# Performance work log

Measured on AMD Instinct MI355X. Metric: run time of the kernel, lower is better.

## Reference

```python
import jax, jax.numpy as jnp
import numpy as np

B, S, D, H = 2, 2048, 2048, 16
DH = D // H  # 128
ROPE_BASE = 10000.0


def setup_inputs() -> dict:
    key = jax.random.key(0)
    ks = jax.random.split(key, 5)
    scale = 0.02
    return {
        "x": jax.random.normal(ks[0], (B, S, D), dtype=jnp.float32),
        "wq": jax.random.normal(ks[1], (D, D), dtype=jnp.float32) * scale,
        "wk": jax.random.normal(ks[2], (D, D), dtype=jnp.float32) * scale,
        "wv": jax.random.normal(ks[3], (D, D), dtype=jnp.float32) * scale,
        "wo": jax.random.normal(ks[4], (D, D), dtype=jnp.float32) * scale,
    }


def _rope_cache(seq_len, dhead):
    # flash-attn RotaryEmbedding: inv_freq over even dims, full rotary_dim = dhead
    inv_freq = 1.0 / (ROPE_BASE ** (jnp.arange(0, dhead, 2, dtype=jnp.float32) / dhead))
    t = jnp.arange(seq_len, dtype=jnp.float32)
    freqs = jnp.einsum("s,d->sd", t, inv_freq)  # [S, DH/2]
    return jnp.cos(freqs), jnp.sin(freqs)


def _apply_rope_interleaved(t, cos, sin):
    # t: [B, S, H, DH]; interleaved pairs (t[...,0::2], t[...,1::2])
    te, to = t[..., 0::2], t[..., 1::2]
    c = cos[None, :, None, :]
    s = sin[None, :, None, :]
    re = te * c - to * s
    ro = te * s + to * c
    return jnp.stack([re, ro], axis=-1).reshape(t.shape)


def reference(x, wq, wk, wv, wo):
    b, s, d = x.shape
    q = (x @ wq).reshape(b, s, H, DH)
    k = (x @ wk).reshape(b, s, H, DH)
    v = (x @ wv).reshape(b, s, H, DH)

    cos, sin = _rope_cache(s, DH)
    q = _apply_rope_interleaved(q.astype(jnp.float32), cos, sin)
    k = _apply_rope_interleaved(k.astype(jnp.float32), cos, sin)

    # flash_attn_func(causal=True) semantics: bf16 inputs, fp32 softmax, scale 1/sqrt(dhead)
    qb = q.astype(jnp.bfloat16)
    kb = k.astype(jnp.bfloat16)
    vb = v.astype(jnp.bfloat16)
    scale = 1.0 / np.sqrt(DH)
    scores = jnp.einsum("bqhd,bkhd->bhqk", qb, kb,
                        preferred_element_type=jnp.float32) * scale
    causal = jnp.tril(jnp.ones((s, s), dtype=bool))
    scores = jnp.where(causal[None, None], scores, -jnp.inf)
    p = jax.nn.softmax(scores, axis=-1)  # fp32
    attn = jnp.einsum("bhqk,bkhd->bqhd", p.astype(jnp.bfloat16), vb,
                      preferred_element_type=jnp.float32)
    attn = attn.astype(jnp.bfloat16).astype(x.dtype)  # flash returns bf16, then .to(x)
    out = attn.reshape(b, s, d) @ wo
    return out
```

## Files before the change

### kernel.cpp

```cpp
#include <hip/hip_runtime.h>
#include <hip/hip_bf16.h>
#include <stdint.h>

#define B_SZ   2
#define S_LEN  2048
#define DMODEL 2048
#define NH     16
#define DHD    128

typedef __attribute__((ext_vector_type(8))) __bf16 bf16x8;
typedef __attribute__((ext_vector_type(4))) float  f32x4;
typedef __attribute__((ext_vector_type(4))) float  float4v;
typedef __attribute__((ext_vector_type(8))) unsigned short ushort8;
typedef __attribute__((ext_vector_type(4))) unsigned short ushort4v;

__device__ __forceinline__ unsigned short f2bf(float f) {
  unsigned int u = __float_as_uint(f);
  unsigned int r = (u + 0x7fffu + ((u >> 16) & 1u)) >> 16;
  return (unsigned short)r;
}

__device__ __forceinline__ unsigned int cvt_pk_bf16(float lo, float hi) {
  unsigned int r;
  asm("v_cvt_pk_bf16_f32 %0, %1, %2" : "=v"(r) : "v"(lo), "v"(hi));
  return r;
}

__device__ __forceinline__ void async_cp16(void* lds, const void* g) {
  __builtin_amdgcn_global_load_lds(
      (const __attribute__((address_space(1))) void*)g,
      (__attribute__((address_space(3))) void*)lds, 16, 0, 0);
}

__global__ __launch_bounds__(256) void k_prep(const float* __restrict__ in,
                                              unsigned short* __restrict__ out,
                                              float* __restrict__ cosT,
                                              float* __restrict__ sinT) {
  const int bx = blockIdx.x;
  const int t = threadIdx.x;
  if (bx < 8192) {
    int i = bx * 256 + t;
    float4v v = ((const float4v*)in)[i];
    ushort4v o;
    o[0] = f2bf(v[0]); o[1] = f2bf(v[1]); o[2] = f2bf(v[2]); o[3] = f2bf(v[3]);
    ((ushort4v*)out)[i] = o;
  } else {
    int i = (bx - 8192) * 256 + t;
    int s = i >> 6, dj = i & 63;
    float e = __expf(-9.210340371976184f * (float)dj * (1.0f / 64.0f));
    float f = (float)s * e;
    cosT[i] = cosf(f);
    sinT[i] = sinf(f);
  }
}

__global__ __launch_bounds__(256) void k_transpose_all(const float* __restrict__ w0,
                                                       const float* __restrict__ w1,
                                                       const float* __restrict__ w2,
                                                       const float* __restrict__ w3,
                                                       unsigned short* __restrict__ WTbase) {
  __shared__ unsigned short tile[64 * 72];
  const int z = blockIdx.z;
  const float* W = (z == 0) ? w0 : (z == 1) ? w1 : (z == 2) ? w2 : w3;
  unsigned short* WT = WTbase + (size_t)z * 4194304;
  const int n0 = blockIdx.x * 64;
  const int k0 = blockIdx.y * 64;
  const int t = threadIdx.x;
#pragma unroll
  for (int i = 0; i < 4; ++i) {
    int c = t + 256 * i;
    int r = c >> 4, c4 = c & 15;
    float4v v = *(const float4v*)(W + (size_t)(k0 + r) * DMODEL + n0 + c4 * 4);
    ushort4v o;
    o[0] = f2bf(v[0]); o[1] = f2bf(v[1]); o[2] = f2bf(v[2]); o[3] = f2bf(v[3]);
    *(ushort4v*)(&tile[r * 72 + c4 * 4]) = o;
  }
  __syncthreads();
#pragma unroll
  for (int i = 0; i < 2; ++i) {
    int c = t + 256 * i;
    int n = c >> 3, k8 = c & 7;
    ushort8 o;
#pragma unroll
    for (int j = 0; j < 8; ++j) o[j] = tile[(k8 * 8 + j) * 72 + n];
    *(ushort8*)(WT + (size_t)(n0 + n) * DMODEL + k0 + k8 * 8) = o;
  }
}

template <int EPI>
__global__ __launch_bounds__(512, 2) void k_gemm128(
    const unsigned short* __restrict__ A,
    const unsigned short* __restrict__ BT,
    float* __restrict__ C0,
    unsigned short* __restrict__ Cq,
    unsigned short* __restrict__ Ck,
    unsigned short* __restrict__ Cv,
    const float* __restrict__ cosT,
    const float* __restrict__ sinT,
    int chn) {
  __shared__ char smem[98304];
  const int tid = threadIdx.x;

  const int xcd = blockIdx.x & 7;
  const int idx = blockIdx.x >> 3;
  const int bm = (xcd >> 2) * 16 + (idx & 15);
  const int bn = (xcd & 3) * chn + (idx >> 4);

  const int gs = (tid & 7) ^ ((tid >> 3) & 7);
  const unsigned short* Abase = A + (size_t)(bm * 128 + (tid >> 3)) * 2048 + gs * 8;
  const unsigned short* Bbase = BT + (size_t)(bn * 256 + (tid >> 3)) * 2048 + gs * 8;
  const int dstA = tid * 16;
  const int dstB = 16384 + tid * 16;

  const int lane = tid & 63, wid = tid >> 6;
  const int wr = wid >> 2, wcn = wid & 3;
  const int lr = lane & 15, hi = lane >> 4;
  int aoff[4][2], boff[4][2];
#pragma unroll
  for (int m = 0; m < 4; ++m) {
    int row = wr * 64 + m * 16 + lr;
#pragma unroll
    for (int k = 0; k < 2; ++k)
      aoff[m][k] = row * 128 + ((((k * 4 + hi)) ^ (row & 7)) << 4);
  }
#pragma unroll
  for (int n = 0; n < 4; ++n) {
    int row = wcn * 64 + n * 16 + lr;
#pragma unroll
    for (int k = 0; k < 2; ++k)
      boff[n][k] = 16384 + row * 128 + ((((k * 4 + hi)) ^ (row & 7)) << 4);
  }

  f32x4 acc[4][4];
#pragma unroll
  for (int m = 0; m < 4; ++m)
#pragma unroll
    for (int n = 0; n < 4; ++n) {
      f32x4 z = {0.f, 0.f, 0.f, 0.f};
      acc[m][n] = z;
    }

#define STG_A(c, t_) do {                                                   \
    const unsigned short* _s = Abase + (t_) * 64;                           \
    async_cp16(smem + (c) * 49152 + dstA, _s);                              \
    async_cp16(smem + (c) * 49152 + dstA + 8192, _s + 64 * 2048);           \
  } while (0)
#define STG_B(c, t_) do {                                                   \
    const unsigned short* _s = Bbase + (t_) * 64;                           \
    async_cp16(smem + (c) * 49152 + dstB, _s);                              \
    async_cp16(smem + (c) * 49152 + dstB + 8192, _s + 64 * 2048);           \
    async_cp16(smem + (c) * 49152 + dstB + 16384, _s + 128 * 2048);         \
    async_cp16(smem + (c) * 49152 + dstB + 24576, _s + 192 * 2048);         \
  } while (0)

  auto tile = [&](int T, int CC, bool DO_A, bool DO_B, int VM) __attribute__((always_inline)) {
    const char* Sb = smem + CC * 49152;
    bf16x8 a0[4], b0[4], a1[4], b1[4];
#pragma unroll
    for (int m = 0; m < 4; ++m) a0[m] = *(const bf16x8*)(Sb + aoff[m][0]);
#pragma unroll
    for (int n = 0; n < 4; ++n) b0[n] = *(const bf16x8*)(Sb + boff[n][0]);
    if (DO_A) STG_A(CC ^ 1, T + 1);
    asm volatile("s_waitcnt lgkmcnt(0)" ::: "memory");
    __builtin_amdgcn_sched_barrier(0);
    __builtin_amdgcn_s_setprio(1);
#pragma unroll
    for (int m = 0; m < 4; ++m) {
      acc[m][0] = __builtin_amdgcn_mfma_f32_16x16x32_bf16(a0[m], b0[0], acc[m][0], 0, 0, 0);
      acc[m][1] = __builtin_amdgcn_mfma_f32_16x16x32_bf16(a0[m], b0[1], acc[m][1], 0, 0, 0);
    }
    __builtin_amdgcn_s_setprio(0);
    __builtin_amdgcn_sched_barrier(0);
#pragma unroll
    for (int m = 0; m < 4; ++m) a1[m] = *(const bf16x8*)(Sb + aoff[m][1]);
#pragma unroll
    for (int n = 0; n < 4; ++n) b1[n] = *(const bf16x8*)(Sb + boff[n][1]);
    __builtin_amdgcn_sched_barrier(0);
    __builtin_amdgcn_s_setprio(1);
#pragma unroll
    for (int m = 0; m < 4; ++m) {
      acc[m][2] = __builtin_amdgcn_mfma_f32_16x16x32_bf16(a0[m], b0[2], acc[m][2], 0, 0, 0);
      acc[m][3] = __builtin_amdgcn_mfma_f32_16x16x32_bf16(a0[m], b0[3], acc[m][3], 0, 0, 0);
    }
    __builtin_amdgcn_s_setprio(0);
    __builtin_amdgcn_s_barrier();
    __builtin_amdgcn_sched_barrier(0);
    asm volatile("s_waitcnt lgkmcnt(0)" ::: "memory");
    __builtin_amdgcn_sched_barrier(0);
    if (DO_B) STG_B(CC, T + 2);
    __builtin_amdgcn_s_setprio(1);
#pragma unroll
    for (int m = 0; m < 4; ++m)
#pragma unroll
      for (int n = 0; n < 4; ++n)
        acc[m][n] = __builtin_amdgcn_mfma_f32_16x16x32_bf16(a1[m], b1[n], acc[m][n], 0, 0, 0);
    __builtin_amdgcn_s_setprio(0);
    if (VM == 0) asm volatile("s_waitcnt vmcnt(4)" ::: "memory");
    else if (VM == 1) asm volatile("s_waitcnt vmcnt(0)" ::: "memory");
    if (VM != 2) {
      __builtin_amdgcn_s_barrier();
      __builtin_amdgcn_sched_barrier(0);
    }
  };

  STG_B(0, 0);
  STG_A(0, 0);
  STG_B(1, 1);
  asm volatile("s_waitcnt vmcnt(4)" ::: "memory");
  __builtin_amdgcn_s_barrier();
  __builtin_amdgcn_sched_barrier(0);

  for (int it = 0; it < 15; ++it) {
    tile(2 * it, 0, true, true, 0);
    tile(2 * it + 1, 1, true, true, 0);
  }
  tile(30, 0, true, false, 1);
  tile(31, 1, false, false, 2);

  const int row_b = bm * 128 + wr * 64 + hi * 4;
  const int col_b = bn * 256 + wcn * 64 + lr;
  if (EPI == 0) {
#pragma unroll
    for (int m = 0; m < 4; ++m)
#pragma unroll
      for (int n = 0; n < 4; ++n) {
        int col = col_b + n * 16;
#pragma unroll
        for (int j = 0; j < 4; ++j) {
          int row = row_b + m * 16 + j;
          C0[(size_t)row * 2048 + col] = acc[m][n][j];
        }
      }
  } else {
    const int sel = bn >> 3;
#pragma unroll
    for (int m = 0; m < 4; ++m) {
#pragma unroll
      for (int n = 0; n < 4; ++n) {
        int col = col_b + n * 16;
        int hh = (col >> 7) & 15, d = col & 127;
        if (sel == 2) {
#pragma unroll
          for (int j = 0; j < 4; ++j) {
            int row = row_b + m * 16 + j;
            int b = row >> 11, s = row & 2047;
            Cv[((size_t)(b * NH + hh) * S_LEN + s) * DHD + d] = f2bf(acc[m][n][j]);
          }
        } else {
          unsigned short* dst = sel ? Ck : Cq;
          int dj = d >> 1;
          float sgn = (d & 1) ? 1.f : -1.f;
#pragma unroll
          for (int j = 0; j < 4; ++j) {
            int row = row_b + m * 16 + j;
            int b = row >> 11, s = row & 2047;
            float v = acc[m][n][j];
            float pp = __shfl_xor(v, 1);
            float cc = cosT[(s << 6) + dj];
            float sn = sinT[(s << 6) + dj];
            dst[((size_t)(b * NH + hh) * S_LEN + s) * DHD + d] = f2bf(v * cc + sgn * pp * sn);
          }
        }
      }
    }
  }
#undef STG_A
#undef STG_B
}

__global__ __launch_bounds__(256) void k_flash_attn(const unsigned short* __restrict__ Qg,
                                                    const unsigned short* __restrict__ Kg,
                                                    const unsigned short* __restrict__ Vg,
                                                    unsigned short* __restrict__ Og) {
  __shared__ unsigned short K_lds[2][64 * 128];
  __shared__ unsigned short VT_lds[2][128 * 64];

  const int lid = blockIdx.x;
  const int pq = (lid >> 3) & 15;
  const int hb = ((lid >> 7) << 3) | (lid & 7);
  const int h = hb & 15, b = hb >> 4;

  const int t = threadIdx.x;
  const int lane = t & 63, wave = t >> 6;
  const int hi = lane >> 4, lr = lane & 15;

  const size_t head = (size_t)(b * NH + h) * (size_t)(S_LEN * DHD);
  const unsigned short* Q = Qg + head;
  const unsigned short* Kp = Kg + head;
  const unsigned short* Vp = Vg + head;

  const int kr0 = t >> 4;
  const int kgc = (t & 15) ^ (kr0 & 7);
  const unsigned short* Kbase = Kp + (size_t)kr0 * DHD + kgc * 8;
  const int kdst = t * 16;

  const int vdc = t & 15, vsp0 = t >> 4;
  const unsigned short* Vbase = Vp + (size_t)(2 * vsp0) * DHD + vdc * 8;
  const int bo0 = 16 * ((vsp0 >> 1) & 3) + 8 * ((vsp0 >> 3) & 1) + 4 * (vsp0 & 1);

  const float sc = 0.08838834764831845f;

  for (int pass = 0; pass < 2; ++pass) {
    const int qt = (pass == 0) ? pq : (31 - pq);
    const int nt = qt + 1;
    const int qbase = qt * 64 + wave * 16;
    const int qrow = qbase + lr;

    bf16x8 qf[4];
    {
      const unsigned short* qr_ = Q + (size_t)(qbase + lr) * DHD;
#pragma unroll
      for (int kc = 0; kc < 4; ++kc) qf[kc] = *(const bf16x8*)(qr_ + kc * 32 + hi * 8);
    }

    f32x4 of[8];
#pragma unroll
    for (int i = 0; i < 8; ++i) {
      f32x4 z = {0.f, 0.f, 0.f, 0.f};
      of[i] = z;
    }
    float mS = -INFINITY;
    float lsum = 0.f;

    {
#pragma unroll
      for (int i = 0; i < 4; ++i)
        async_cp16((char*)K_lds[0] + kdst + i * 4096, Kbase + (size_t)(16 * i) * DHD);
      ushort8 va0 = *(const ushort8*)(Vbase);
      ushort8 vb0 = *(const ushort8*)(Vbase + DHD);
      ushort8 va1 = *(const ushort8*)(Vbase + (size_t)32 * DHD);
      ushort8 vb1 = *(const ushort8*)(Vbase + (size_t)33 * DHD);
#pragma unroll
      for (int j = 0; j < 8; ++j) {
        int row = vdc * 8 + j;
        int swz = ((j ^ vdc) & 7) << 4;
        *(unsigned int*)((char*)VT_lds[0] + row * 128 + (bo0 ^ swz)) =
            (unsigned int)va0[j] | ((unsigned int)vb0[j] << 16);
        *(unsigned int*)((char*)VT_lds[0] + row * 128 + ((bo0 | 64) ^ swz)) =
            (unsigned int)va1[j] | ((unsigned int)vb1[j] << 16);
      }
    }
    __syncthreads();

    for (int tt = 0; tt < nt; ++tt) {
      const int cur = tt & 1;
      const int kv0 = tt * 64;
      const bool more = (tt + 1 < nt);
      const bool diag = (tt == qt);

      ushort8 va0, vb0, va1, vb1;
      if (more) {
        const unsigned short* ks = Kbase + (size_t)(kv0 + 64) * DHD;
#pragma unroll
        for (int i = 0; i < 4; ++i)
          async_cp16((char*)K_lds[cur ^ 1] + kdst + i * 4096, ks + (size_t)(16 * i) * DHD);
        const unsigned short* vs = Vbase + (size_t)(kv0 + 64) * DHD;
        va0 = *(const ushort8*)(vs);
        vb0 = *(const ushort8*)(vs + DHD);
        va1 = *(const ushort8*)(vs + (size_t)32 * DHD);
        vb1 = *(const ushort8*)(vs + (size_t)33 * DHD);
      }

      const char* Kb = (const char*)K_lds[cur];
      f32x4 sf[4];
#pragma unroll
      for (int n = 0; n < 4; ++n) {
        f32x4 z = {0.f, 0.f, 0.f, 0.f};
        sf[n] = z;
      }
      __builtin_amdgcn_s_setprio(1);
#pragma unroll
      for (int n = 0; n < 4; ++n) {
        const int kr = n * 16 + lr;
        const int kswz = (kr & 7) << 4;
#pragma unroll
        for (int kc = 0; kc < 4; ++kc) {
          bf16x8 kf = *(const bf16x8*)(Kb + kr * 256 + ((kc * 64 + hi * 16) ^ kswz));
          sf[n] = __builtin_amdgcn_mfma_f32_16x16x32_bf16(kf, qf[kc], sf[n], 0, 0, 0);
        }
      }
      __builtin_amdgcn_s_setprio(0);

      float p[4][4];
      float mx = -INFINITY;
      if (diag) {
#pragma unroll
        for (int n = 0; n < 4; ++n)
#pragma unroll
          for (int j = 0; j < 4; ++j) {
            int kvcol = kv0 + n * 16 + hi * 4 + j;
            float v = (kvcol > qrow) ? -INFINITY : sf[n][j];
            p[n][j] = v;
            mx = fmaxf(mx, v);
          }
      } else {
#pragma unroll
        for (int n = 0; n < 4; ++n)
#pragma unroll
          for (int j = 0; j < 4; ++j) {
            float v = sf[n][j];
            p[n][j] = v;
            mx = fmaxf(mx, v);
          }
      }
      mx = fmaxf(mx, __shfl_xor(mx, 16));
      mx = fmaxf(mx, __shfl_xor(mx, 32));
      float mn = fmaxf(mS, mx);
      float corr = __expf((mS - mn) * sc);
      mS = mn;
      float mns = mn * sc;
      float rs = 0.f;
#pragma unroll
      for (int n = 0; n < 4; ++n)
#pragma unroll
        for (int j = 0; j < 4; ++j) {
          float e = __expf(__builtin_fmaf(p[n][j], sc, -mns));
          p[n][j] = e;
          rs += e;
        }
      rs += __shfl_xor(rs, 16);
      rs += __shfl_xor(rs, 32);
      lsum = lsum * corr + rs;

      unsigned int pk[4][2];
#pragma unroll
      for (int n = 0; n < 4; ++n) {
        pk[n][0] = cvt_pk_bf16(p[n][0], p[n][1]);
        pk[n][1] = cvt_pk_bf16(p[n][2], p[n][3]);
      }

      float corrb[4];
#pragma unroll
      for (int j = 0; j < 4; ++j) corrb[j] = __shfl(corr, hi * 4 + j);
#pragma unroll
      for (int nd = 0; nd < 8; ++nd)
#pragma unroll
        for (int j = 0; j < 4; ++j) of[nd][j] *= corrb[j];

      const char* Vb = (const char*)VT_lds[cur];
      __builtin_amdgcn_s_setprio(1);
#pragma unroll
      for (int kc = 0; kc < 2; ++kc) {
        union { unsigned int u[4]; bf16x8 v; } pa;
        pa.u[0] = pk[2 * kc][0];
        pa.u[1] = pk[2 * kc][1];
        pa.u[2] = pk[2 * kc + 1][0];
        pa.u[3] = pk[2 * kc + 1][1];
#pragma unroll
        for (int nd = 0; nd < 8; ++nd) {
          const int vr = nd * 16 + lr;
          const int vswz = ((vr & 7) ^ ((vr >> 3) & 7)) << 4;
          bf16x8 vf = *(const bf16x8*)(Vb + vr * 128 + ((kc * 64 + hi * 16) ^ vswz));
          of[nd] = __builtin_amdgcn_mfma_f32_16x16x32_bf16(pa.v, vf, of[nd], 0, 0, 0);
        }
      }
      __builtin_amdgcn_s_setprio(0);

      if (more) {
        char* Vw = (char*)VT_lds[cur ^ 1];
#pragma unroll
        for (int j = 0; j < 8; ++j) {
          int row = vdc * 8 + j;
          int swz = ((j ^ vdc) & 7) << 4;
          *(unsigned int*)(Vw + row * 128 + (bo0 ^ swz)) =
              (unsigned int)va0[j] | ((unsigned int)vb0[j] << 16);
          *(unsigned int*)(Vw + row * 128 + ((bo0 | 64) ^ swz)) =
              (unsigned int)va1[j] | ((unsigned int)vb1[j] << 16);
        }
      }
      __syncthreads();
    }

    float inv[4];
#pragma unroll
    for (int j = 0; j < 4; ++j) {
      float ls = __shfl(lsum, hi * 4 + j);
      inv[j] = 1.0f / ls;
    }
#pragma unroll
    for (int nd = 0; nd < 8; ++nd)
#pragma unroll
      for (int j = 0; j < 4; ++j) {
        int qr = qbase + hi * 4 + j;
        Og[((size_t)(b * S_LEN + qr) * NH + h) * DHD + nd * 16 + lr] = f2bf(of[nd][j] * inv[j]);
      }
  }
}

extern "C" void kernel_launch(void* const* d_in, const int* in_sizes, int n_in,
                              void* d_out, int out_size, void* d_ws, size_t ws_size,
                              hipStream_t stream) {
  const float* x  = (const float*)d_in[0];
  const float* wq = (const float*)d_in[1];
  const float* wk = (const float*)d_in[2];
  const float* wv = (const float*)d_in[3];
  const float* wo = (const float*)d_in[4];
  float* out = (float*)d_out;

  char* ws = (char*)d_ws;
  unsigned short* xb    = (unsigned short*)(ws);
  unsigned short* wqT   = (unsigned short*)(ws + 16777216);
  unsigned short* woT   = (unsigned short*)(ws + 41943040);
  unsigned short* qb    = (unsigned short*)(ws + 50331648);
  unsigned short* kb    = (unsigned short*)(ws + 67108864);
  unsigned short* vb    = (unsigned short*)(ws + 83886080);
  float*          cosT  = (float*)(ws + 100663296);
  float*          sinT  = (float*)(ws + 101187584);
  unsigned short* attnb = xb;

  k_prep<<<8704, 256, 0, stream>>>(x, xb, cosT, sinT);
  dim3 tg(32, 32, 4);
  k_transpose_all<<<tg, 256, 0, stream>>>(wq, wk, wv, wo, wqT);

  k_gemm128<1><<<768, 512, 0, stream>>>(xb, wqT, nullptr, qb, kb, vb, cosT, sinT, 6);

  k_flash_attn<<<512, 256, 0, stream>>>(qb, kb, vb, attnb);

  k_gemm128<0><<<256, 512, 0, stream>>>(attnb, woT, out, nullptr, nullptr, nullptr,
                                        nullptr, nullptr, 2);
}
```

Measured before the change: 229.1 us.

## Use 256x384 tiles for QKV GEMM and merge prep with weight transpose

New measurement: 238.4 us. +4.0%, slower.

```diff
diff --git a/kernel.cpp b/kernel.cpp
--- a/kernel.cpp
+++ b/kernel.cpp
@@ -32,20 +32,52 @@
       (__attribute__((address_space(3))) void*)lds, 16, 0, 0);
 }
 
-__global__ __launch_bounds__(256) void k_prep(const float* __restrict__ in,
-                                              unsigned short* __restrict__ out,
-                                              float* __restrict__ cosT,
-                                              float* __restrict__ sinT) {
+__global__ __launch_bounds__(256) void k_prep_all(const float* __restrict__ x,
+                                                  const float* __restrict__ w0,
+                                                  const float* __restrict__ w1,
+                                                  const float* __restrict__ w2,
+                                                  const float* __restrict__ w3,
+                                                  unsigned short* __restrict__ xb,
+                                                  unsigned short* __restrict__ WTbase,
+                                                  float* __restrict__ cosT,
+                                                  float* __restrict__ sinT) {
+  __shared__ unsigned short tile[64 * 72];
   const int bx = blockIdx.x;
   const int t = threadIdx.x;
-  if (bx < 8192) {
-    int i = bx * 256 + t;
-    float4v v = ((const float4v*)in)[i];
+  if (bx < 4096) {
+    const int z = bx >> 10;
+    const int wi = bx & 1023;
+    const float* W = (z == 0) ? w0 : (z == 1) ? w1 : (z == 2) ? w2 : w3;
+    unsigned short* WT = WTbase + (size_t)z * 4194304;
+    const int n0 = (wi & 31) * 64;
+    const int k0 = (wi >> 5) * 64;
+#pragma unroll
+    for (int i = 0; i < 4; ++i) {
+      int c = t + 256 * i;
+      int r = c >> 4, c4 = c & 15;
+      float4v v = *(const float4v*)(W + (size_t)(k0 + r) * DMODEL + n0 + c4 * 4);
+      ushort4v o;
+      o[0] = f2bf(v[0]); o[1] = f2bf(v[1]); o[2] = f2bf(v[2]); o[3] = f2bf(v[3]);
+      *(ushort4v*)(&tile[r * 72 + c4 * 4]) = o;
+    }
+    __syncthreads();
+#pragma unroll
+    for (int i = 0; i < 2; ++i) {
+      int c = t + 256 * i;
+      int n = c >> 3, k8 = c & 7;
+      ushort8 o;
+#pragma unroll
+      for (int j = 0; j < 8; ++j) o[j] = tile[(k8 * 8 + j) * 72 + n];
+      *(ushort8*)(WT + (size_t)(n0 + n) * DMODEL + k0 + k8 * 8) = o;
+    }
+  } else if (bx < 12288) {
+    int i = (bx - 4096) * 256 + t;
+    float4v v = ((const float4v*)x)[i];
     ushort4v o;
     o[0] = f2bf(v[0]); o[1] = f2bf(v[1]); o[2] = f2bf(v[2]); o[3] = f2bf(v[3]);
-    ((ushort4v*)out)[i] = o;
+    ((ushort4v*)xb)[i] = o;
   } else {
-    int i = (bx - 8192) * 256 + t;
+    int i = (bx - 12288) * 256 + t;
     int s = i >> 6, dj = i & 63;
     float e = __expf(-9.210340371976184f * (float)dj * (1.0f / 64.0f));
     float f = (float)s * e;
@@ -54,49 +86,150 @@
   }
 }
 
-__global__ __launch_bounds__(256) void k_transpose_all(const float* __restrict__ w0,
-                                                       const float* __restrict__ w1,
-                                                       const float* __restrict__ w2,
-                                                       const float* __restrict__ w3,
-                                                       unsigned short* __restrict__ WTbase) {
-  __shared__ unsigned short tile[64 * 72];
-  const int z = blockIdx.z;
-  const float* W = (z == 0) ? w0 : (z == 1) ? w1 : (z == 2) ? w2 : w3;
-  unsigned short* WT = WTbase + (size_t)z * 4194304;
-  const int n0 = blockIdx.x * 64;
-  const int k0 = blockIdx.y * 64;
-  const int t = threadIdx.x;
-#pragma unroll
-  for (int i = 0; i < 4; ++i) {
-    int c = t + 256 * i;
-    int r = c >> 4, c4 = c & 15;
-    float4v v = *(const float4v*)(W + (size_t)(k0 + r) * DMODEL + n0 + c4 * 4);
-    ushort4v o;
-    o[0] = f2bf(v[0]); o[1] = f2bf(v[1]); o[2] = f2bf(v[2]); o[3] = f2bf(v[3]);
-    *(ushort4v*)(&tile[r * 72 + c4 * 4]) = o;
-  }
-  __syncthreads();
-#pragma unroll
-  for (int i = 0; i < 2; ++i) {
-    int c = t + 256 * i;
-    int n = c >> 3, k8 = c & 7;
-    ushort8 o;
-#pragma unroll
-    for (int j = 0; j < 8; ++j) o[j] = tile[(k8 * 8 + j) * 72 + n];
-    *(ushort8*)(WT + (size_t)(n0 + n) * DMODEL + k0 + k8 * 8) = o;
-  }
-}
-
-template <int EPI>
-__global__ __launch_bounds__(512, 2) void k_gemm128(
+__global__ __launch_bounds__(512, 1) void k_gemm_qkv(
     const unsigned short* __restrict__ A,
     const unsigned short* __restrict__ BT,
-    float* __restrict__ C0,
     unsigned short* __restrict__ Cq,
     unsigned short* __restrict__ Ck,
     unsigned short* __restrict__ Cv,
     const float* __restrict__ cosT,
-    const float* __restrict__ sinT,
+    const float* __restrict__ sinT) {
+  __shared__ char smem[122880];
+  const int tid = threadIdx.x;
+
+  const int xcd = blockIdx.x & 7;
+  const int idx = blockIdx.x >> 3;
+  const int bm = (xcd >> 1) * 4 + (idx & 3);
+  const int bn = (xcd & 1) * 8 + (idx >> 2);
+
+  const int r0 = tid >> 2;
+  const int gs = (tid & 3) ^ (r0 & 3);
+  const unsigned short* Abase = A + (size_t)(bm * 256 + r0) * 2048 + gs * 8;
+  const unsigned short* Bbase = BT + (size_t)(bn * 384 + r0) * 2048 + gs * 8;
+  const int dstA = tid * 16;
+  const int dstB = 16384 + tid * 16;
+
+  const int lane = tid & 63, wid = tid >> 6;
+  const int wr = wid >> 2, wcn = wid & 3;
+  const int lr = lane & 15, hi = lane >> 4;
+  const int swz = (hi ^ (lr & 3)) << 4;
+  const int aB = (wr * 128 + lr) * 64 + swz;
+  const int bB = 16384 + (wcn * 96 + lr) * 64 + swz;
+
+  f32x4 acc[8][6];
+#pragma unroll
+  for (int m = 0; m < 8; ++m)
+#pragma unroll
+    for (int n = 0; n < 6; ++n) {
+      f32x4 z = {0.f, 0.f, 0.f, 0.f};
+      acc[m][n] = z;
+    }
+
+#define STG(c, t_) do {                                                     \
+    const unsigned short* _a = Abase + (t_) * 32;                           \
+    async_cp16(smem + (c) * 40960 + dstA, _a);                              \
+    async_cp16(smem + (c) * 40960 + dstA + 8192, _a + (size_t)128 * 2048);  \
+    const unsigned short* _b = Bbase + (t_) * 32;                           \
+    async_cp16(smem + (c) * 40960 + dstB, _b);                              \
+    async_cp16(smem + (c) * 40960 + dstB + 8192, _b + (size_t)128 * 2048);  \
+    async_cp16(smem + (c) * 40960 + dstB + 16384, _b + (size_t)256 * 2048); \
+  } while (0)
+
+  auto tile = [&](int T, int CC) __attribute__((always_inline)) {
+    const char* Sb = smem + CC * 40960;
+    if (T + 2 < 64) {
+      const int nc = (CC + 2 >= 3) ? (CC - 1) : (CC + 2);
+      STG(nc, T + 2);
+    }
+    bf16x8 b0[6], a0[4];
+#pragma unroll
+    for (int n = 0; n < 6; ++n) b0[n] = *(const bf16x8*)(Sb + bB + n * 1024);
+#pragma unroll
+    for (int m = 0; m < 4; ++m) a0[m] = *(const bf16x8*)(Sb + aB + m * 1024);
+    asm volatile("s_waitcnt lgkmcnt(0)" ::: "memory");
+    __builtin_amdgcn_sched_barrier(0);
+    __builtin_amdgcn_s_setprio(1);
+#pragma unroll
+    for (int m = 0; m < 4; ++m)
+#pragma unroll
+      for (int n = 0; n < 6; ++n)
+        acc[m][n] = __builtin_amdgcn_mfma_f32_16x16x32_bf16(a0[m], b0[n], acc[m][n], 0, 0, 0);
+    __builtin_amdgcn_s_setprio(0);
+    __builtin_amdgcn_sched_barrier(0);
+    bf16x8 a1[4];
+#pragma unroll
+    for (int m = 0; m < 4; ++m) a1[m] = *(const bf16x8*)(Sb + aB + (m + 4) * 1024);
+    asm volatile("s_waitcnt lgkmcnt(0)" ::: "memory");
+    __builtin_amdgcn_sched_barrier(0);
+    __builtin_amdgcn_s_setprio(1);
+#pragma unroll
+    for (int m = 0; m < 4; ++m)
+#pragma unroll
+      for (int n = 0; n < 6; ++n)
+        acc[m + 4][n] = __builtin_amdgcn_mfma_f32_16x16x32_bf16(a1[m], b0[n], acc[m + 4][n], 0, 0, 0);
+    __builtin_amdgcn_s_setprio(0);
+    if (T < 62) asm volatile("s_waitcnt vmcnt(5)" ::: "memory");
+    else if (T == 62) asm volatile("s_waitcnt vmcnt(0)" ::: "memory");
+    if (T < 63) {
+      __builtin_amdgcn_s_barrier();
+      __builtin_amdgcn_sched_barrier(0);
+    }
+  };
+
+  STG(0, 0);
+  STG(1, 1);
+  asm volatile("s_waitcnt vmcnt(5)" ::: "memory");
+  __builtin_amdgcn_s_barrier();
+  __builtin_amdgcn_sched_barrier(0);
+
+  for (int it = 0; it < 21; ++it) {
+    tile(3 * it, 0);
+    tile(3 * it + 1, 1);
+    tile(3 * it + 2, 2);
+  }
+  tile(63, 0);
+
+  const int row_b = bm * 256 + wr * 128 + hi * 4;
+  const int col_b = bn * 384 + wcn * 96 + lr;
+#pragma unroll
+  for (int n = 0; n < 6; ++n) {
+    const int col = col_b + n * 16;
+    const int sel = col >> 11;
+    const int hh = (col >> 7) & 15, d = col & 127;
+    if (sel == 2) {
+#pragma unroll
+      for (int m = 0; m < 8; ++m)
+#pragma unroll
+        for (int j = 0; j < 4; ++j) {
+          int row = row_b + m * 16 + j;
+          int b = row >> 11, s = row & 2047;
+          Cv[((size_t)(b * NH + hh) * S_LEN + s) * DHD + d] = f2bf(acc[m][n][j]);
+        }
+    } else {
+      unsigned short* dst = sel ? Ck : Cq;
+      const int dj = d >> 1;
+      const float sgn = (d & 1) ? 1.f : -1.f;
+#pragma unroll
+      for (int m = 0; m < 8; ++m)
+#pragma unroll
+        for (int j = 0; j < 4; ++j) {
+          int row = row_b + m * 16 + j;
+          int b = row >> 11, s = row & 2047;
+          float v = acc[m][n][j];
+          float pp = __shfl_xor(v, 1);
+          float cc = cosT[(s << 6) + dj];
+          float sn = sinT[(s << 6) + dj];
+          dst[((size_t)(b * NH + hh) * S_LEN + s) * DHD + d] = f2bf(v * cc + sgn * pp * sn);
+        }
+    }
+  }
+#undef STG
+}
+
+__global__ __launch_bounds__(512, 2) void k_gemm_wo(
+    const unsigned short* __restrict__ A,
+    const unsigned short* __restrict__ BT,
+    float* __restrict__ C0,
     int chn) {
   __shared__ char smem[98304];
   const int tid = threadIdx.x;
@@ -219,51 +352,17 @@
 
   const int row_b = bm * 128 + wr * 64 + hi * 4;
   const int col_b = bn * 256 + wcn * 64 + lr;
-  if (EPI == 0) {
-#pragma unroll
-    for (int m = 0; m < 4; ++m)
-#pragma unroll
-      for (int n = 0; n < 4; ++n) {
-        int col = col_b + n * 16;
-#pragma unroll
-        for (int j = 0; j < 4; ++j) {
-          int row = row_b + m * 16 + j;
-          C0[(size_t)row * 2048 + col] = acc[m][n][j];
-        }
-      }
-  } else {
-    const int sel = bn >> 3;
-#pragma unroll
-    for (int m = 0; m < 4; ++m) {
-#pragma unroll
-      for (int n = 0; n < 4; ++n) {
-        int col = col_b + n * 16;
-        int hh = (col >> 7) & 15, d = col & 127;
-        if (sel == 2) {
-#pragma unroll
-          for (int j = 0; j < 4; ++j) {
-            int row = row_b + m * 16 + j;
-            int b = row >> 11, s = row & 2047;
-            Cv[((size_t)(b * NH + hh) * S_LEN + s) * DHD + d] = f2bf(acc[m][n][j]);
-          }
-        } else {
-          unsigned short* dst = sel ? Ck : Cq;
-          int dj = d >> 1;
-          float sgn = (d & 1) ? 1.f : -1.f;
-#pragma unroll
-          for (int j = 0; j < 4; ++j) {
-            int row = row_b + m * 16 + j;
-            int b = row >> 11, s = row & 2047;
-            float v = acc[m][n][j];
-            float pp = __shfl_xor(v, 1);
-            float cc = cosT[(s << 6) + dj];
-            float sn = sinT[(s << 6) + dj];
-            dst[((size_t)(b * NH + hh) * S_LEN + s) * DHD + d] = f2bf(v * cc + sgn * pp * sn);
-          }
-        }
-      }
-    }
-  }
+#pragma unroll
+  for (int m = 0; m < 4; ++m)
+#pragma unroll
+    for (int n = 0; n < 4; ++n) {
+      int col = col_b + n * 16;
+#pragma unroll
+      for (int j = 0; j < 4; ++j) {
+        int row = row_b + m * 16 + j;
+        C0[(size_t)row * 2048 + col] = acc[m][n][j];
+      }
+    }
 #undef STG_A
 #undef STG_B
 }
@@ -508,14 +607,11 @@
   float*          sinT  = (float*)(ws + 101187584);
   unsigned short* attnb = xb;
 
-  k_prep<<<8704, 256, 0, stream>>>(x, xb, cosT, sinT);
-  dim3 tg(32, 32, 4);
-  k_transpose_all<<<tg, 256, 0, stream>>>(wq, wk, wv, wo, wqT);
-
-  k_gemm128<1><<<768, 512, 0, stream>>>(xb, wqT, nullptr, qb, kb, vb, cosT, sinT, 6);
+  k_prep_all<<<12800, 256, 0, stream>>>(x, wq, wk, wv, wo, xb, wqT, cosT, sinT);
+
+  k_gemm_qkv<<<256, 512, 0, stream>>>(xb, wqT, qb, kb, vb, cosT, sinT);
 
   k_flash_attn<<<512, 256, 0, stream>>>(qb, kb, vb, attnb);
 
-  k_gemm128<0><<<256, 512, 0, stream>>>(attnb, woT, out, nullptr, nullptr, nullptr,
-                                        nullptr, nullptr, 2);
-}
+  k_gemm_wo<<<256, 512, 0, stream>>>(attnb, woT, out, 2);
+}
```

## Store V transposed from QKV GEMM and async-load it into LDS; merge prep kernels

Applied to the files above, without the earlier changes.

Result: slower. 283.0 us (+23.5%).

```diff
diff --git a/kernel.cpp b/kernel.cpp
--- a/kernel.cpp
+++ b/kernel.cpp
@@ -32,58 +32,63 @@
       (__attribute__((address_space(3))) void*)lds, 16, 0, 0);
 }
 
-__global__ __launch_bounds__(256) void k_prep(const float* __restrict__ in,
-                                              unsigned short* __restrict__ out,
-                                              float* __restrict__ cosT,
-                                              float* __restrict__ sinT) {
+__device__ __forceinline__ void async_cp4(void* lds, const void* g) {
+  __builtin_amdgcn_global_load_lds(
+      (const __attribute__((address_space(1))) void*)g,
+      (__attribute__((address_space(3))) void*)lds, 4, 0, 0);
+}
+
+__global__ __launch_bounds__(256) void k_prep_all(const float* __restrict__ x,
+                                                  const float* __restrict__ w0,
+                                                  const float* __restrict__ w1,
+                                                  const float* __restrict__ w2,
+                                                  const float* __restrict__ w3,
+                                                  unsigned short* __restrict__ xb,
+                                                  unsigned short* __restrict__ WTbase,
+                                                  float* __restrict__ cosT,
+                                                  float* __restrict__ sinT) {
+  __shared__ unsigned short tile[64 * 72];
   const int bx = blockIdx.x;
   const int t = threadIdx.x;
-  if (bx < 8192) {
-    int i = bx * 256 + t;
-    float4v v = ((const float4v*)in)[i];
+  if (bx < 4096) {
+    const int z = bx >> 10;
+    const int wi = bx & 1023;
+    const float* W = (z == 0) ? w0 : (z == 1) ? w1 : (z == 2) ? w2 : w3;
+    unsigned short* WT = WTbase + (size_t)z * 4194304;
+    const int n0 = (wi & 31) * 64;
+    const int k0 = (wi >> 5) * 64;
+#pragma unroll
+    for (int i = 0; i < 4; ++i) {
+      int c = t + 256 * i;
+      int r = c >> 4, c4 = c & 15;
+      float4v v = *(const float4v*)(W + (size_t)(k0 + r) * DMODEL + n0 + c4 * 4);
+      ushort4v o;
+      o[0] = f2bf(v[0]); o[1] = f2bf(v[1]); o[2] = f2bf(v[2]); o[3] = f2bf(v[3]);
+      *(ushort4v*)(&tile[r * 72 + c4 * 4]) = o;
+    }
+    __syncthreads();
+#pragma unroll
+    for (int i = 0; i < 2; ++i) {
+      int c = t + 256 * i;
+      int n = c >> 3, k8 = c & 7;
+      ushort8 o;
+#pragma unroll
+      for (int j = 0; j < 8; ++j) o[j] = tile[(k8 * 8 + j) * 72 + n];
+      *(ushort8*)(WT + (size_t)(n0 + n) * DMODEL + k0 + k8 * 8) = o;
+    }
+  } else if (bx < 12288) {
+    int i = (bx - 4096) * 256 + t;
+    float4v v = ((const float4v*)x)[i];
     ushort4v o;
     o[0] = f2bf(v[0]); o[1] = f2bf(v[1]); o[2] = f2bf(v[2]); o[3] = f2bf(v[3]);
-    ((ushort4v*)out)[i] = o;
+    ((ushort4v*)xb)[i] = o;
   } else {
-    int i = (bx - 8192) * 256 + t;
+    int i = (bx - 12288) * 256 + t;
     int s = i >> 6, dj = i & 63;
     float e = __expf(-9.210340371976184f * (float)dj * (1.0f / 64.0f));
     float f = (float)s * e;
     cosT[i] = cosf(f);
     sinT[i] = sinf(f);
-  }
-}
-
-__global__ __launch_bounds__(256) void k_transpose_all(const float* __restrict__ w0,
-                                                       const float* __restrict__ w1,
-                                                       const float* __restrict__ w2,
-                                                       const float* __restrict__ w3,
-                                                       unsigned short* __restrict__ WTbase) {
-  __shared__ unsigned short tile[64 * 72];
-  const int z = blockIdx.z;
-  const float* W = (z == 0) ? w0 : (z == 1) ? w1 : (z == 2) ? w2 : w3;
-  unsigned short* WT = WTbase + (size_t)z * 4194304;
-  const int n0 = blockIdx.x * 64;
-  const int k0 = blockIdx.y * 64;
-  const int t = threadIdx.x;
-#pragma unroll
-  for (int i = 0; i < 4; ++i) {
-    int c = t + 256 * i;
-    int r = c >> 4, c4 = c & 15;
-    float4v v = *(const float4v*)(W + (size_t)(k0 + r) * DMODEL + n0 + c4 * 4);
-    ushort4v o;
-    o[0] = f2bf(v[0]); o[1] = f2bf(v[1]); o[2] = f2bf(v[2]); o[3] = f2bf(v[3]);
-    *(ushort4v*)(&tile[r * 72 + c4 * 4]) = o;
-  }
-  __syncthreads();
-#pragma unroll
-  for (int i = 0; i < 2; ++i) {
-    int c = t + 256 * i;
-    int n = c >> 3, k8 = c & 7;
-    ushort8 o;
-#pragma unroll
-    for (int j = 0; j < 8; ++j) o[j] = tile[(k8 * 8 + j) * 72 + n];
-    *(ushort8*)(WT + (size_t)(n0 + n) * DMODEL + k0 + k8 * 8) = o;
   }
 }
 
@@ -240,12 +245,14 @@
         int col = col_b + n * 16;
         int hh = (col >> 7) & 15, d = col & 127;
         if (sel == 2) {
-#pragma unroll
-          for (int j = 0; j < 4; ++j) {
-            int row = row_b + m * 16 + j;
-            int b = row >> 11, s = row & 2047;
-            Cv[((size_t)(b * NH + hh) * S_LEN + s) * DHD + d] = f2bf(acc[m][n][j]);
-          }
+          int row0 = row_b + m * 16;
+          int b = row0 >> 11, s0 = row0 & 2047;
+          ushort4v w4;
+          w4[0] = f2bf(acc[m][n][0]);
+          w4[1] = f2bf(acc[m][n][1]);
+          w4[2] = f2bf(acc[m][n][2]);
+          w4[3] = f2bf(acc[m][n][3]);
+          *(ushort4v*)(Cv + ((size_t)((b * NH + hh) * DHD + d)) * S_LEN + s0) = w4;
         } else {
           unsigned short* dst = sel ? Ck : Cq;
           int dj = d >> 1;
@@ -287,16 +294,25 @@
   const size_t head = (size_t)(b * NH + h) * (size_t)(S_LEN * DHD);
   const unsigned short* Q = Qg + head;
   const unsigned short* Kp = Kg + head;
-  const unsigned short* Vp = Vg + head;
+  const unsigned short* Vt = Vg + head;
 
   const int kr0 = t >> 4;
   const int kgc = (t & 15) ^ (kr0 & 7);
   const unsigned short* Kbase = Kp + (size_t)kr0 * DHD + kgc * 8;
   const int kdst = t * 16;
 
-  const int vdc = t & 15, vsp0 = t >> 4;
-  const unsigned short* Vbase = Vp + (size_t)(2 * vsp0) * DHD + vdc * 8;
-  const int bo0 = 16 * ((vsp0 >> 1) & 3) + 8 * ((vsp0 >> 3) & 1) + 4 * (vsp0 & 1);
+  int voffs[16];
+#pragma unroll
+  for (int i = 0; i < 16; ++i) {
+    int row = 32 * wave + 2 * i + (lane >> 5);
+    int W = (lane & 31) * 4;
+    int vs = ((row & 7) ^ ((row >> 3) & 7)) << 4;
+    int Lb = W ^ vs;
+    int s0 = Lb >> 1;
+    int kap = 32 * (s0 >> 5) + 16 * ((s0 >> 2) & 1) + 4 * ((s0 >> 3) & 3) + (s0 & 3);
+    voffs[i] = row * S_LEN + kap;
+  }
+  const int vdst0 = wave * 4096 + (lane & 63) * 4;
 
   const float sc = 0.08838834764831845f;
 
@@ -326,19 +342,9 @@
 #pragma unroll
       for (int i = 0; i < 4; ++i)
         async_cp16((char*)K_lds[0] + kdst + i * 4096, Kbase + (size_t)(16 * i) * DHD);
-      ushort8 va0 = *(const ushort8*)(Vbase);
-      ushort8 vb0 = *(const ushort8*)(Vbase + DHD);
-      ushort8 va1 = *(const ushort8*)(Vbase + (size_t)32 * DHD);
-      ushort8 vb1 = *(const ushort8*)(Vbase + (size_t)33 * DHD);
-#pragma unroll
-      for (int j = 0; j < 8; ++j) {
-        int row = vdc * 8 + j;
-        int swz = ((j ^ vdc) & 7) << 4;
-        *(unsigned int*)((char*)VT_lds[0] + row * 128 + (bo0 ^ swz)) =
-            (unsigned int)va0[j] | ((unsigned int)vb0[j] << 16);
-        *(unsigned int*)((char*)VT_lds[0] + row * 128 + ((bo0 | 64) ^ swz)) =
-            (unsigned int)va1[j] | ((unsigned int)vb1[j] << 16);
-      }
+#pragma unroll
+      for (int i = 0; i < 16; ++i)
+        async_cp4((char*)VT_lds[0] + vdst0 + i * 256, Vt + voffs[i]);
     }
     __syncthreads();
 
@@ -348,17 +354,15 @@
       const bool more = (tt + 1 < nt);
       const bool diag = (tt == qt);
 
-      ushort8 va0, vb0, va1, vb1;
       if (more) {
         const unsigned short* ks = Kbase + (size_t)(kv0 + 64) * DHD;
 #pragma unroll
         for (int i = 0; i < 4; ++i)
           async_cp16((char*)K_lds[cur ^ 1] + kdst + i * 4096, ks + (size_t)(16 * i) * DHD);
-        const unsigned short* vs = Vbase + (size_t)(kv0 + 64) * DHD;
-        va0 = *(const ushort8*)(vs);
-        vb0 = *(const ushort8*)(vs + DHD);
-        va1 = *(const ushort8*)(vs + (size_t)32 * DHD);
-        vb1 = *(const ushort8*)(vs + (size_t)33 * DHD);
+        const unsigned short* vs = Vt + (kv0 + 64);
+#pragma unroll
+        for (int i = 0; i < 16; ++i)
+          async_cp4((char*)VT_lds[cur ^ 1] + vdst0 + i * 256, vs + voffs[i]);
       }
 
       const char* Kb = (const char*)K_lds[cur];
@@ -456,18 +460,6 @@
       }
       __builtin_amdgcn_s_setprio(0);
 
-      if (more) {
-        char* Vw = (char*)VT_lds[cur ^ 1];
-#pragma unroll
-        for (int j = 0; j < 8; ++j) {
-          int row = vdc * 8 + j;
-          int swz = ((j ^ vdc) & 7) << 4;
-          *(unsigned int*)(Vw + row * 128 + (bo0 ^ swz)) =
-              (unsigned int)va0[j] | ((unsigned int)vb0[j] << 16);
-          *(unsigned int*)(Vw + row * 128 + ((bo0 | 64) ^ swz)) =
-              (unsigned int)va1[j] | ((unsigned int)vb1[j] << 16);
-        }
-      }
       __syncthreads();
     }
 
@@ -508,9 +500,7 @@
   float*          sinT  = (float*)(ws + 101187584);
   unsigned short* attnb = xb;
 
-  k_prep<<<8704, 256, 0, stream>>>(x, xb, cosT, sinT);
-  dim3 tg(32, 32, 4);
-  k_transpose_all<<<tg, 256, 0, stream>>>(wq, wk, wv, wo, wqT);
+  k_prep_all<<<12800, 256, 0, stream>>>(x, wq, wk, wv, wo, xb, wqT, cosT, sinT);
 
   k_gemm128<1><<<768, 512, 0, stream>>>(xb, wqT, nullptr, qb, kb, vb, cosT, sinT, 6);
 
```
